# Performance work log

Hardware: AMD Instinct MI355X
Metric: run time of the kernel (lower is better)

The kernel has to match this reference:

```python
import jax, jax.numpy as jnp
import numpy as np

B, N, K, D, H, W = 16, 32, 32, 64, 128, 128  # batch, instances, dot_number, dot_dimension, fmap HxW
IMAGE_SIZE = 512.0
DOWN = 4.0
HID = 128


def setup_inputs() -> dict:
    key = jax.random.key(0)
    ks = jax.random.split(key, 16)
    s = 0.05
    x = jax.random.normal(ks[0], (B, 64, H, W), jnp.float32)
    mask_point = jax.random.uniform(ks[1], (B, N, K, 2), jnp.float32) * 511.0  # image-space coords
    point_mask = jnp.ones((B, N, K), jnp.int32)  # 1 = real point, 0 = zero-padded
    return {
        "x": x,
        "mask_point": mask_point,
        "point_mask": point_mask,
        "conv1_w": jax.random.normal(ks[2], (64, 64, 3, 3), jnp.float32) * s,
        "conv1_b": jnp.zeros((64,), jnp.float32),
        "conv2_w": jax.random.normal(ks[3], (D, 64), jnp.float32) * s,
        "conv2_b": jnp.full((D,), -2.19, jnp.float32),  # bias_fill with bias_value
        "Wih_e": jax.random.normal(ks[4], (4 * HID, D), jnp.float32) * s,
        "Whh_e": jax.random.normal(ks[5], (4 * HID, HID), jnp.float32) * s,
        "bih_e": jnp.zeros((4 * HID,), jnp.float32),
        "bhh_e": jnp.zeros((4 * HID,), jnp.float32),
        "Wih_d": jax.random.normal(ks[6], (4 * HID, HID), jnp.float32) * s,
        "Whh_d": jax.random.normal(ks[7], (4 * HID, HID), jnp.float32) * s,
        "bih_d": jnp.zeros((4 * HID,), jnp.float32),
        "bhh_d": jnp.zeros((4 * HID,), jnp.float32),
        "W1": jax.random.normal(ks[8], (64, HID), jnp.float32) * s,
        "b1": jnp.zeros((64,), jnp.float32),
        "W2": jax.random.normal(ks[9], (2, 64), jnp.float32) * s,
        "b2": jnp.zeros((2,), jnp.float32),
    }


def _lstm(seq, Wih, Whh, bih, bhh, h0, c0):
    # seq: [T, Bflat, in]; PyTorch gate order i, f, g, o
    bias = bih + bhh
    def step(carry, xt):
        h, c = carry
        g = xt @ Wih.T + h @ Whh.T + bias
        i, f, gg, o = jnp.split(g, 4, axis=-1)
        c = jax.nn.sigmoid(f) * c + jax.nn.sigmoid(i) * jnp.tanh(gg)
        h = jax.nn.sigmoid(o) * jnp.tanh(c)
        return (h, c), h
    (hT, cT), ys = jax.lax.scan(step, (h0, c0), seq)
    return ys, (hT, cT)


def reference(x, mask_point, point_mask, conv1_w, conv1_b, conv2_w, conv2_b,
              Wih_e, Whh_e, bih_e, bhh_e, Wih_d, Whh_d, bih_d, bhh_d,
              W1, b1, W2, b2):
    # SingleHead extraction: 3x3 conv -> ReLU -> 1x1 conv
    feat = jax.lax.conv_general_dilated(
        x, conv1_w, (1, 1), 'SAME',
        dimension_numbers=('NCHW', 'OIHW', 'NCHW')) + conv1_b[None, :, None, None]
    feat = jax.nn.relu(feat)
    fmap = jnp.einsum('bchw,dc->bdhw', feat, conv2_w) + conv2_b[None, :, None, None]
    xf = fmap.reshape(B, D, H * W)

    # keypoint index math (vectorized version of the nested python loops)
    pts = jnp.minimum(mask_point / DOWN, 127.0)        # [B,N,K,2] feature-map coords
    gt = pts * DOWN                                     # gt_keypoints
    flat = (pts[..., 1] * (IMAGE_SIZE / DOWN) + pts[..., 0]).astype(jnp.int32)  # [B,N,K]

    # gather dot features; zero padding where point_mask == 0
    dots = jax.vmap(lambda f, idx: f.T[idx])(xf, flat)  # [B,N,K,D]
    dots = dots * point_mask[..., None].astype(dots.dtype)

    seq = dots.reshape(B * N, K, D).transpose(1, 0, 2)  # [K, B*N, D] (time-major)
    h0 = jnp.zeros((B * N, HID), seq.dtype)
    enc, (h, c) = _lstm(seq, Wih_e, Whh_e, bih_e, bhh_e, h0, h0)
    dec, _ = _lstm(enc, Wih_d, Whh_d, bih_d, bhh_d, h, c)

    y = jax.nn.relu(dec @ W1.T + b1) @ W2.T + b2        # [K, B*N, 2]
    kp = y.transpose(1, 0, 2).reshape(B, N, K, 2)
    return kp, gt
```

## Files before the change

### kernel.cpp

```cpp
#include <hip/hip_runtime.h>
#include <stdint.h>

#define NSEQ 512
#define HIDN 128

#define OFF_FEIH   0
#define OFF_BIAS_E 65536
#define OFF_BIAS_D 67584
#define OFF_W1P    69632
#define OFF_W2P    143360
#define OFF_FLAT   151552
#define OFF_W1H    217088
#define OFF_FEHH   233472
#define OFF_FDIH8  364544
#define OFF_FDHH8  430080
#define OFF_W2T    495616
#define OFF_W1F8   504832
#define OFF_DOTS   (1024*1024)
#define OFF_XT     (4*1024*1024)
#define WS_NEED_XT ((size_t)(4*1024*1024) + (size_t)16*128*128*64 + 1024)

typedef _Float16 h2f __attribute__((ext_vector_type(2)));
typedef _Float16 f16x8 __attribute__((ext_vector_type(8)));
typedef float    f32x4 __attribute__((ext_vector_type(4)));

static __device__ __forceinline__ h2f u2h(uint32_t u) {
  union { uint32_t u; h2f h; } v; v.u = u; return v.h;
}

#if __has_builtin(__builtin_amdgcn_fdot2)
static __device__ __forceinline__ float fdot2_(uint32_t a, uint32_t b, float c) {
  return __builtin_amdgcn_fdot2(u2h(a), u2h(b), c, false);
}
#else
static __device__ __forceinline__ float fdot2_(uint32_t a, uint32_t b, float c) {
  h2f x = u2h(a), y = u2h(b);
  return c + (float)x.x * (float)y.x + (float)x.y * (float)y.y;
}
#endif

static __device__ __forceinline__ uint32_t packh(float a, float b) {
  union { _Float16 h[2]; uint32_t u; } v;
  v.h[0] = (_Float16)a; v.h[1] = (_Float16)b; return v.u;
}
static __device__ __forceinline__ float sig_(float x) {
  return 1.0f / (1.0f + __expf(-x));
}
static __device__ __forceinline__ float tanh_(float x) {
  return 1.0f - 2.0f / (1.0f + __expf(2.0f * x));
}

static __device__ __forceinline__ uint32_t f2e4m3_sw(float f) {
  union { float f; uint32_t u; } v; v.f = f;
  uint32_t s = (v.u >> 24) & 0x80u;
  float af = fabsf(f);
  if (af == 0.0f) return s;
  if (af >= 448.0f) return s | 0x7Eu;
  int e; float m = frexpf(af, &e);
  int E = e + 6;
  float mant = m * 2.0f - 1.0f;
  int mm = (int)(mant * 8.0f + 0.5f);
  if (mm == 8) { mm = 0; ++E; }
  if (E < 1) {
    int sm = (int)(af * 512.0f + 0.5f);
    return s | (uint32_t)(sm > 7 ? 7 : sm);
  }
  if (E > 15) return s | 0x7Eu;
  return s | ((uint32_t)E << 3) | (uint32_t)mm;
}
static __device__ __forceinline__ uint32_t pk4_fp8(float a, float b, float c, float d) {
#if __has_builtin(__builtin_amdgcn_cvt_pk_fp8_f32)
  int r = __builtin_amdgcn_cvt_pk_fp8_f32(a, b, 0, false);
  r = __builtin_amdgcn_cvt_pk_fp8_f32(c, d, r, true);
  return (uint32_t)r;
#else
  return f2e4m3_sw(a) | (f2e4m3_sw(b) << 8) | (f2e4m3_sw(c) << 16) | (f2e4m3_sw(d) << 24);
#endif
}
static __device__ __forceinline__ uint8_t f8_(float v) {
#if __has_builtin(__builtin_amdgcn_cvt_pk_fp8_f32)
  return (uint8_t)(__builtin_amdgcn_cvt_pk_fp8_f32(v, 0.f, 0, false) & 0xFF);
#else
  return (uint8_t)f2e4m3_sw(v);
#endif
}
static __device__ __forceinline__ long u2l(uint2 v) {
  union { uint2 v; long l; } x; x.v = v; return x.l;
}
static __device__ __forceinline__ uint2 ldg_frag8(const uint2* p) {
  uint2 r;
  asm volatile("global_load_dwordx2 %0, %1, off" : "=v"(r) : "v"(p));
  return r;
}
static __device__ __forceinline__ void frag_fence() {
  asm volatile("s_waitcnt vmcnt(0)" ::: "memory");
  __builtin_amdgcn_sched_barrier(0);
}

static __device__ void prep_body(int idx,
    const float* Wih_e, const float* Whh_e,
    const float* bih_e, const float* bhh_e,
    const float* Wih_d, const float* Whh_d,
    const float* bih_d, const float* bhh_d,
    const float* w1, const float* w2, const float* W1,
    const float* mask_point, float* out_gt, int* flat,
    char* ws, int w1_order) {
  float*    bias_e = (float*)(ws + OFF_BIAS_E);
  float*    bias_d = (float*)(ws + OFF_BIAS_D);
  uint32_t* w1p    = (uint32_t*)(ws + OFF_W1P);
  uint32_t* w2p    = (uint32_t*)(ws + OFF_W2P);
  uint32_t* W1h    = (uint32_t*)(ws + OFF_W1H);
  uint32_t* w2t    = (uint32_t*)(ws + OFF_W2T);
  uint32_t* w1f8   = (uint32_t*)(ws + OFF_W1F8);

  if (idx < 16384) {
    int j2 = idx & 3, lane = (idx >> 2) & 63, kt = (idx >> 8) & 1, gt = idx >> 9;
    int g = gt*16 + (lane & 15);
    int k = kt*32 + ((lane >> 4) & 3)*8 + 2*j2;
    ((uint32_t*)(ws + OFF_FEIH))[idx] = packh(Wih_e[g*64 + k], Wih_e[g*64 + k + 1]);
    return;
  }
  idx -= 16384;
  if (idx < 512) { bias_e[idx] = bih_e[idx] + bhh_e[idx]; return; }
  idx -= 512;
  if (idx < 512) { bias_d[idx] = bih_d[idx] + bhh_d[idx]; return; }
  idx -= 512;
  if (idx < 288*64) {
    int i2 = idx >> 6, c = idx & 63;
    if (w1_order) {
      int tap = i2 >> 5, cin = (i2 & 31) * 2;
      w1p[idx] = packh(w1[c*576 + cin*9 + tap], w1[c*576 + (cin+1)*9 + tap]);
    } else {
      w1p[idx] = packh(w1[c*576 + 2*i2], w1[c*576 + 2*i2 + 1]);
    }
    return;
  }
  idx -= 288*64;
  if (idx < 32*64) {
    int c2 = idx >> 6, d = idx & 63;
    w2p[idx] = packh(w2[d*64 + 2*c2], w2[d*64 + 2*c2 + 1]);
    return;
  }
  idx -= 32*64;
  if (idx < 64*64) {
    int k2 = idx >> 6, j = idx & 63;
    W1h[idx] = packh(W1[j*128 + 2*k2], W1[j*128 + 2*k2 + 1]);
    return;
  }
  idx -= 64*64;
  if (idx < 32768) {
    int j2 = idx & 3, lane = (idx >> 2) & 63, kt = (idx >> 8) & 3, gt = idx >> 10;
    int g = gt*16 + (lane & 15);
    int k = kt*32 + ((lane >> 4) & 3)*8 + 2*j2;
    ((uint32_t*)(ws + OFF_FEHH))[idx] = packh(Whh_e[g*128 + k], Whh_e[g*128 + k + 1]);
    return;
  }
  idx -= 32768;
  if (idx < 16384) {
    int half = idx & 1, lane = (idx >> 1) & 63, kt = (idx >> 7) & 3, gt = idx >> 9;
    int g = gt*16 + (lane & 15);
    int kb = kt*32 + ((lane >> 4) & 3)*8 + half*4;
    const float* W = Wih_d;
    ((uint32_t*)(ws + OFF_FDIH8))[(((gt*4 + kt)*64 + lane) << 1) | half] =
        pk4_fp8(W[g*128 + kb], W[g*128 + kb + 1], W[g*128 + kb + 2], W[g*128 + kb + 3]);
    return;
  }
  idx -= 16384;
  if (idx < 16384) {
    int half = idx & 1, lane = (idx >> 1) & 63, kt = (idx >> 7) & 3, gt = idx >> 9;
    int g = gt*16 + (lane & 15);
    int kb = kt*32 + ((lane >> 4) & 3)*8 + half*4;
    const float* W = Whh_d;
    ((uint32_t*)(ws + OFF_FDHH8))[(((gt*4 + kt)*64 + lane) << 1) | half] =
        pk4_fp8(W[g*128 + kb], W[g*128 + kb + 1], W[g*128 + kb + 2], W[g*128 + kb + 3]);
    return;
  }
  idx -= 16384;
  if (idx < 64*36) {
    int d = idx / 36, c2 = idx - (idx/36)*36;
    w2t[idx] = (c2 < 32) ? packh(w2[d*64 + 2*c2], w2[d*64 + 2*c2 + 1]) : 0u;
    return;
  }
  idx -= 64*36;
  if (idx < 64*144) {
    int c = idx / 144, j = idx - (idx/144)*144;
    int tap = j >> 4, cin0 = (j & 15) * 4;
    w1f8[idx] = pk4_fp8(w1[c*576 + (cin0+0)*9 + tap] * 16.0f,
                        w1[c*576 + (cin0+1)*9 + tap] * 16.0f,
                        w1[c*576 + (cin0+2)*9 + tap] * 16.0f,
                        w1[c*576 + (cin0+3)*9 + tap] * 16.0f);
    return;
  }
  idx -= 64*144;
  if (idx < 16384) {
    float mx = mask_point[idx*2 + 0];
    float my = mask_point[idx*2 + 1];
    float fx = fminf(mx * 0.25f, 127.0f);
    float fy = fminf(my * 0.25f, 127.0f);
    out_gt[idx*2 + 0] = fx * 4.0f;
    out_gt[idx*2 + 1] = fy * 4.0f;
    flat[idx] = (int)(__fmaf_rn(fy, 128.0f, fx));
    return;
  }
}
#define PREP_TOTAL (16384 + 512 + 512 + 288*64 + 32*64 + 64*64 + 32768 + 16384 + 16384 + 64*36 + 64*144 + 16384)
#define PREP_BLOCKS ((PREP_TOTAL + 255) / 256)

__global__ __launch_bounds__(256) void prep_kernel(
    const float* Wih_e, const float* Whh_e, const float* bih_e, const float* bhh_e,
    const float* Wih_d, const float* Whh_d, const float* bih_d, const float* bhh_d,
    const float* w1, const float* w2, const float* W1,
    const float* mask_point, float* out_gt, int* flat, char* ws, int w1_order) {
  prep_body(blockIdx.x * 256 + threadIdx.x,
            Wih_e, Whh_e, bih_e, bhh_e, Wih_d, Whh_d, bih_d, bhh_d,
            w1, w2, W1, mask_point, out_gt, flat, ws, w1_order);
}

__global__ __launch_bounds__(256, 2) void transpose_prep_kernel(
    const float* x, uint32_t* xT8,
    const float* Wih_e, const float* Whh_e, const float* bih_e, const float* bhh_e,
    const float* Wih_d, const float* Whh_d, const float* bih_d, const float* bhh_d,
    const float* w1, const float* w2, const float* W1,
    const float* mask_point, float* out_gt, int* flat, char* ws) {
  __shared__ float lds[64][257];
  int bid = blockIdx.x;
  if (bid >= 1024) {
    prep_body((bid - 1024) * 256 + threadIdx.x,
              Wih_e, Whh_e, bih_e, bhh_e, Wih_d, Whh_d, bih_d, bhh_d,
              w1, w2, W1, mask_point, out_gt, flat, ws, 1);
    return;
  }
  int xt = bid & 3, yt = (bid >> 2) & 15, b = bid >> 6;
  int x0 = xt * 32, y0 = yt * 8;
  int tx = threadIdx.x & 31, ty = threadIdx.x >> 5;
  #pragma unroll 8
  for (int c = 0; c < 64; ++c)
    lds[c][ty*32 + tx] = x[((b*64 + c)*128 + (y0 + ty))*128 + (x0 + tx)];
  __syncthreads();
  #pragma unroll 8
  for (int r = 0; r < 16; ++r) {
    int i = threadIdx.x + 256*r;
    int c4 = i & 15, pos = i >> 4;
    int yy = pos >> 5, xx = pos & 31;
    uint32_t v = pk4_fp8(lds[c4*4+0][pos], lds[c4*4+1][pos],
                         lds[c4*4+2][pos], lds[c4*4+3][pos]);
    xT8[((b*128 + y0 + yy)*128 + (x0 + xx))*16 + c4] = v;
  }
}

__global__ __launch_bounds__(512, 2) void conv_mfma8_kernel(
    const uint32_t* xT8, const int* point_mask,
    const float* conv1_b, const float* conv2_b,
    const char* ws_ro, _Float16* dots_h, const int* flat) {
  __shared__ __attribute__((aligned(16))) uint32_t w1s8[64*146];
  __shared__ __attribute__((aligned(16))) uint32_t patch8[32*146];
  __shared__ __attribute__((aligned(16))) uint32_t t1s[32*36];

  const uint32_t* w1f8 = (const uint32_t*)(ws_ro + OFF_W1F8);
  const uint32_t* w2t  = (const uint32_t*)(ws_ro + OFF_W2T);
  int tid  = threadIdx.x;
  int lane = tid & 63, wave = tid >> 6;
  int r = wave & 3, g = wave >> 2;
  int cl = lane & 15, lgrp = lane >> 4;

  #pragma unroll
  for (int i = tid; i < 64*144; i += 512) {
    int c = i / 144, j = i - c*144;
    w1s8[c*146 + j] = w1f8[i];
  }

  uint4 a2[2];
  #pragma unroll
  for (int kt = 0; kt < 2; ++kt)
    a2[kt] = *(const uint4*)&w2t[(r*16 + cl)*36 + kt*16 + lgrp*4];

  float4 b1r = *(const float4*)&conv1_b[r*16 + lgrp*4];
  float4 b2v = *(const float4*)&conv2_b[r*16 + lgrp*4];
  f32x4 b1v = {b1r.x*16.f, b1r.y*16.f, b1r.z*16.f, b1r.w*16.f};

  for (int it = 0; it < 2; ++it) {
    int p0 = blockIdx.x * 64 + it * 32;
    __syncthreads();
    #pragma unroll
    for (int rr = 0; rr < 9; ++rr) {
      int u = tid + 512*rr;
      int slot = u / 144, j = u - slot*144;
      int tap = j >> 4, c4 = j & 15;
      int p = p0 + slot;
      int fl = flat[p];
      int hh = fl >> 7, ww = fl & 127;
      int b = p >> 10;
      int dy = tap / 3, dx = tap - dy*3;
      int yy = hh + dy - 1, xx = ww + dx - 1;
      uint32_t v = 0u;
      if (yy >= 0 && yy < 128 && xx >= 0 && xx < 128)
        v = xT8[((b*128 + yy)*128 + xx)*16 + c4];
      patch8[slot*146 + j] = v;
    }
    __syncthreads();

    f32x4 acc = b1v;
    #pragma unroll
    for (int kt = 0; kt < 18; ++kt) {
      long af = u2l(*(const uint2*)&w1s8[(r*16 + cl)*146 + kt*8 + lgrp*2]);
      long bf = u2l(*(const uint2*)&patch8[(g*16 + cl)*146 + kt*8 + lgrp*2]);
      acc = __builtin_amdgcn_mfma_f32_16x16x32_fp8_fp8(af, bf, acc, 0, 0, 0);
    }
    {
      int trow = (g*16 + cl)*36 + r*8 + lgrp*2;
      t1s[trow]     = packh(fmaxf(acc[0], 0.f) * 0.0625f, fmaxf(acc[1], 0.f) * 0.0625f);
      t1s[trow + 1] = packh(fmaxf(acc[2], 0.f) * 0.0625f, fmaxf(acc[3], 0.f) * 0.0625f);
    }
    __syncthreads();

    f32x4 acc2 = {b2v.x, b2v.y, b2v.z, b2v.w};
    #pragma unroll
    for (int kt = 0; kt < 2; ++kt) {
      f16x8 af; __builtin_memcpy(&af, &a2[kt], 16);
      f16x8 bf = *(const f16x8*)&t1s[(g*16 + cl)*36 + kt*16 + lgrp*4];
      acc2 = __builtin_amdgcn_mfma_f32_16x16x32_f16(af, bf, acc2, 0, 0, 0);
    }
    {
      int p = p0 + g*16 + cl;
      float m = (float)point_mask[p];
      int kk = p & 31, bn = p >> 5;
      int d0 = r*16 + lgrp*4;
      uint2 o;
      o.x = packh(acc2[0]*m, acc2[1]*m);
      o.y = packh(acc2[2]*m, acc2[3]*m);
      *(uint2*)&dots_h[(size_t)(kk*NSEQ + bn)*64 + d0] = o;
    }
  }
}

__global__ __launch_bounds__(256, 2) void conv_gather_kernel(
    const float* x, const int* point_mask,
    const float* conv1_b, const float* conv2_b,
    const char* ws_ro, _Float16* dots_h, const int* flat) {
  __shared__ uint32_t w1s[64*292];
  __shared__ uint32_t patch2[4*288];
  __shared__ uint32_t tl2[4*32];

  const uint32_t* w1p = (const uint32_t*)(ws_ro + OFF_W1P);
  const uint32_t* w2p = (const uint32_t*)(ws_ro + OFF_W2P);
  int tid = threadIdx.x;
  for (int i = tid; i < 288*64; i += 256) {
    int i2 = i >> 6, cc = i & 63;
    w1s[cc*292 + i2] = w1p[i];
  }

  int q = tid >> 6, c = tid & 63;
  float c1b = conv1_b[c], c2b = conv2_b[c];

  for (int g = 0; g < 8; ++g) {
    int p0 = blockIdx.x * 32 + g * 4;
    __syncthreads();
    #pragma unroll
    for (int r = 0; r < 9; ++r) {
      int l = tid + 256*r;
      int slot = l / 576;
      int within = l - slot*576;
      int cp = within / 9;
      int tap = within - cp*9;
      int p = p0 + slot;
      int fl = flat[p];
      int hh = fl >> 7, ww = fl & 127;
      int b = p >> 10;
      int yy = hh + tap/3 - 1, xx = ww + tap%3 - 1;
      float v = 0.0f;
      if (yy >= 0 && yy < 128 && xx >= 0 && xx < 128)
        v = x[((b*64 + cp)*128 + yy)*128 + xx];
      ((_Float16*)patch2)[l] = (_Float16)v;
    }
    __syncthreads();

    float a0 = c1b, a1 = 0.f, a2 = 0.f, a3 = 0.f;
    int cbase = c * 292, pbase = q * 288;
    #pragma unroll 4
    for (int i2 = 0; i2 < 288; i2 += 4) {
      a0 = fdot2_(w1s[cbase + i2+0], patch2[pbase + i2+0], a0);
      a1 = fdot2_(w1s[cbase + i2+1], patch2[pbase + i2+1], a1);
      a2 = fdot2_(w1s[cbase + i2+2], patch2[pbase + i2+2], a2);
      a3 = fdot2_(w1s[cbase + i2+3], patch2[pbase + i2+3], a3);
    }
    float t1 = fmaxf((a0 + a1) + (a2 + a3), 0.0f);
    ((_Float16*)tl2)[q*64 + c] = (_Float16)t1;

    float acc2 = c2b;
    #pragma unroll
    for (int c2i = 0; c2i < 32; ++c2i)
      acc2 = fdot2_(w2p[c2i*64 + c], tl2[q*32 + c2i], acc2);
    int p = p0 + q;
    acc2 *= (float)point_mask[p];
    int k = p & 31, bn = p >> 5;
    dots_h[(k*NSEQ + bn)*64 + c] = (_Float16)acc2;
  }
}

__global__ __launch_bounds__(512, 2) void lstm_head_kernel(
    const char* ws_ro,
    const float* b1, const float* W2, const float* b2,
    float* out_kp) {
  const f16x8* feih   = (const f16x8*)(ws_ro + OFF_FEIH);
  const f16x8* fehh   = (const f16x8*)(ws_ro + OFF_FEHH);
  const uint2* fdih8  = (const uint2*)(ws_ro + OFF_FDIH8);
  const uint2* fdhh8  = (const uint2*)(ws_ro + OFF_FDHH8);
  const float* bias_e = (const float*)(ws_ro + OFF_BIAS_E);
  const float* bias_d = (const float*)(ws_ro + OFF_BIAS_D);
  const uint32_t* dots_u = (const uint32_t*)(ws_ro + OFF_DOTS);
  const uint32_t* W1h = (const uint32_t*)(ws_ro + OFF_W1H);

  __shared__ __attribute__((aligned(16))) uint32_t xs[2][32][32];
  __shared__ __attribute__((aligned(16))) uint32_t enc8[2][32][32];
  __shared__ __attribute__((aligned(16))) uint32_t dech2[2][32][64];
  __shared__ __attribute__((aligned(16))) uint32_t hb2[2][64];
  __shared__ __attribute__((aligned(16))) uint32_t hb8[2][32];
  __shared__ __attribute__((aligned(16))) float    gb[2][512];
  __shared__ float hidf[64][65];

  int tid  = threadIdx.x;
  int lane = tid & 63, wave = tid >> 6;
  int col  = lane & 15, lgrp = lane >> 4;
  int sb   = col & 1;
  int bn0  = blockIdx.x * 2;

  int s_nl = tid >> 7, u_nl = tid & 127;
  float c_reg = 0.0f;

  for (int i = tid; i < 2048; i += 512) {
    int s = i >> 10, rem = i & 1023, t = rem >> 5, k2 = rem & 31;
    xs[s][t][k2] = dots_u[(t*NSEQ + bn0 + s)*32 + k2];
  }

  f16x8 ax[4][2], ae[4][4];
  #pragma unroll
  for (int g0 = 0; g0 < 4; ++g0) {
    #pragma unroll
    for (int kt = 0; kt < 2; ++kt)
      ax[g0][kt] = feih[((wave*4 + g0)*2 + kt)*64 + lane];
    #pragma unroll
    for (int kt = 0; kt < 4; ++kt)
      ae[g0][kt] = fehh[((wave*4 + g0)*4 + kt)*64 + lane];
  }

  float be0 = bias_e[u_nl],       be1 = bias_e[128 + u_nl];
  float be2 = bias_e[256 + u_nl], be3 = bias_e[384 + u_nl];

  if (tid < 128) hb2[tid >> 6][tid & 63] = 0u;
  __syncthreads();

  const f16x8 bzero = {};

  for (int t = 0; t < 32; ++t) {
    f16x8 bx[2], bf[4];
    #pragma unroll
    for (int kt = 0; kt < 2; ++kt)
      bx[kt] = *(const f16x8*)&xs[sb][t][kt*16 + lgrp*4];
    #pragma unroll
    for (int kt = 0; kt < 4; ++kt) {
      if (col < 2) bf[kt] = *(const f16x8*)&hb2[col][kt*16 + lgrp*4];
      else         bf[kt] = bzero;
    }
    #pragma unroll
    for (int g0 = 0; g0 < 4; ++g0) {
      f32x4 acc = {0.f, 0.f, 0.f, 0.f};
      #pragma unroll
      for (int kt = 0; kt < 2; ++kt)
        acc = __builtin_amdgcn_mfma_f32_16x16x32_f16(ax[g0][kt], bx[kt], acc, 0, 0, 0);
      #pragma unroll
      for (int kt = 0; kt < 4; ++kt)
        acc = __builtin_amdgcn_mfma_f32_16x16x32_f16(ae[g0][kt], bf[kt], acc, 0, 0, 0);
      if (col < 2)
        *(f32x4*)&gb[col][(wave*4 + g0)*16 + lgrp*4] = acc;
    }
    __syncthreads();
    if (tid < 256) {
      float ig = sig_ (gb[s_nl][u_nl]       + be0);
      float fg = sig_ (gb[s_nl][128 + u_nl] + be1);
      float gg = tanh_(gb[s_nl][256 + u_nl] + be2);
      float og = sig_ (gb[s_nl][384 + u_nl] + be3);
      c_reg = fg * c_reg + ig * gg;
      float hh = og * tanh_(c_reg);
      ((_Float16*)&hb2[s_nl][0])[u_nl] = (_Float16)hh;
      ((uint8_t*)&enc8[s_nl][t][0])[u_nl] = f8_(hh);
    }
    __syncthreads();
  }

  if (tid < 256) {
    float hv = (float)((_Float16*)&hb2[s_nl][0])[u_nl];
    ((uint8_t*)&hb8[s_nl][0])[u_nl] = f8_(hv);
  }

  uint2 dih8[4][4], dhh8[4][4];
  #pragma unroll
  for (int g0 = 0; g0 < 4; ++g0)
    #pragma unroll
    for (int kt = 0; kt < 4; ++kt) {
      dih8[g0][kt] = ldg_frag8(&fdih8[((wave*4 + g0)*4 + kt)*64 + lane]);
      dhh8[g0][kt] = ldg_frag8(&fdhh8[((wave*4 + g0)*4 + kt)*64 + lane]);
    }
  frag_fence();
  float bdi = 0.f, bdf = 0.f, bdg = 0.f, bdo = 0.f;
  if (tid < 256) {
    bdi = bias_d[u_nl];       bdf = bias_d[128 + u_nl];
    bdg = bias_d[256 + u_nl]; bdo = bias_d[384 + u_nl];
  }
  __syncthreads();

  for (int t = 0; t < 32; ++t) {
    long bx[4], bh[4];
    #pragma unroll
    for (int kt = 0; kt < 4; ++kt) {
      if (col < 2) {
        bx[kt] = u2l(*(const uint2*)&enc8[col][t][kt*8 + lgrp*2]);
        bh[kt] = u2l(*(const uint2*)&hb8[col][kt*8 + lgrp*2]);
      } else { bx[kt] = 0; bh[kt] = 0; }
    }
    #pragma unroll
    for (int g0 = 0; g0 < 4; ++g0) {
      f32x4 acc = {0.f, 0.f, 0.f, 0.f};
      #pragma unroll
      for (int kt = 0; kt < 4; ++kt)
        acc = __builtin_amdgcn_mfma_f32_16x16x32_fp8_fp8(
            u2l(dih8[g0][kt]), bx[kt], acc, 0, 0, 0);
      #pragma unroll
      for (int kt = 0; kt < 4; ++kt)
        acc = __builtin_amdgcn_mfma_f32_16x16x32_fp8_fp8(
            u2l(dhh8[g0][kt]), bh[kt], acc, 0, 0, 0);
      if (col < 2)
        *(f32x4*)&gb[col][(wave*4 + g0)*16 + lgrp*4] = acc;
    }
    __syncthreads();
    if (tid < 256) {
      float ig = sig_ (gb[s_nl][u_nl]       + bdi);
      float fg = sig_ (gb[s_nl][128 + u_nl] + bdf);
      float gg = tanh_(gb[s_nl][256 + u_nl] + bdg);
      float og = sig_ (gb[s_nl][384 + u_nl] + bdo);
      c_reg = fg * c_reg + ig * gg;
      float hh = og * tanh_(c_reg);
      ((uint8_t*)&hb8[s_nl][0])[u_nl] = f8_(hh);
      ((_Float16*)&dech2[s_nl][t][0])[u_nl] = (_Float16)hh;
    }
    __syncthreads();
  }

  {
    int j = tid & 63, w = tid >> 6;
    float acc[8];
    #pragma unroll
    for (int m = 0; m < 8; ++m) acc[m] = b1[j];
    #pragma unroll 8
    for (int k = 0; k < 64; ++k) {
      uint32_t wv = W1h[k*64 + j];
      #pragma unroll
      for (int m = 0; m < 8; ++m) {
        int st = w + 8*m;
        acc[m] = fdot2_(wv, dech2[st >> 5][st & 31][k], acc[m]);
      }
    }
    #pragma unroll
    for (int m = 0; m < 8; ++m) {
      int st = w + 8*m;
      hidf[st][j] = fmaxf(acc[m], 0.0f);
    }
  }
  __syncthreads();
  if (tid < 128) {
    int st = tid >> 1, e = tid & 1;
    float acc = b2[e];
    #pragma unroll 16
    for (int j = 0; j < 64; ++j) acc += W2[e*64 + j] * hidf[st][j];
    int s = st >> 5, t = st & 31;
    out_kp[((bn0 + s)*32 + t)*2 + e] = acc;
  }
}

extern "C" void kernel_launch(void* const* d_in, const int* in_sizes, int n_in,
                              void* d_out, int out_size, void* d_ws, size_t ws_size,
                              hipStream_t stream) {
  const float* x          = (const float*)d_in[0];
  const float* mask_point = (const float*)d_in[1];
  const int*   point_mask = (const int*)d_in[2];
  const float* conv1_w    = (const float*)d_in[3];
  const float* conv1_b    = (const float*)d_in[4];
  const float* conv2_w    = (const float*)d_in[5];
  const float* conv2_b    = (const float*)d_in[6];
  const float* Wih_e      = (const float*)d_in[7];
  const float* Whh_e      = (const float*)d_in[8];
  const float* bih_e      = (const float*)d_in[9];
  const float* bhh_e      = (const float*)d_in[10];
  const float* Wih_d      = (const float*)d_in[11];
  const float* Whh_d      = (const float*)d_in[12];
  const float* bih_d      = (const float*)d_in[13];
  const float* bhh_d      = (const float*)d_in[14];
  const float* W1         = (const float*)d_in[15];
  const float* b1         = (const float*)d_in[16];
  const float* W2         = (const float*)d_in[17];
  const float* b2         = (const float*)d_in[18];

  float* out = (float*)d_out;
  char*  ws  = (char*)d_ws;

  const bool use_xt = (ws_size >= WS_NEED_XT);

  if (use_xt) {
    transpose_prep_kernel<<<1024 + PREP_BLOCKS, 256, 0, stream>>>(
        x, (uint32_t*)(ws + OFF_XT),
        Wih_e, Whh_e, bih_e, bhh_e, Wih_d, Whh_d, bih_d, bhh_d,
        conv1_w, conv2_w, W1, mask_point, out + 32768, (int*)(ws + OFF_FLAT), ws);
    conv_mfma8_kernel<<<256, 512, 0, stream>>>(
        (const uint32_t*)(ws + OFF_XT), point_mask, conv1_b, conv2_b,
        ws, (_Float16*)(ws + OFF_DOTS), (const int*)(ws + OFF_FLAT));
  } else {
    prep_kernel<<<PREP_BLOCKS, 256, 0, stream>>>(
        Wih_e, Whh_e, bih_e, bhh_e, Wih_d, Whh_d, bih_d, bhh_d,
        conv1_w, conv2_w, W1, mask_point, out + 32768, (int*)(ws + OFF_FLAT),
        ws, 1);
    conv_gather_kernel<<<512, 256, 0, stream>>>(
        x, point_mask, conv1_b, conv2_b,
        ws, (_Float16*)(ws + OFF_DOTS), (const int*)(ws + OFF_FLAT));
  }

  lstm_head_kernel<<<256, 512, 0, stream>>>(ws, b1, W2, b2, out);
}
```

Measured before the change: 106.1 us.

## Fuse conv gather kernel with LSTM head kernel, keeping dots in LDS

Merges the fp8 MFMA conv/gather kernel and the LSTM+MLP head into one kernel. Each block computes the 64 dot features for its two sequences and writes them straight into shared memory instead of a global dots buffer, then runs the encoder/decoder LSTM and head. Shared memory regions are aliased between the phases. This removes one kernel launch and the global round trip for the dots tensor, at the cost of higher LDS and register pressure in a single kernel. The LSTM weight fragments are now loaded only after the conv phase rather than overlapped with it.

After: 103.5 us. -2.5%, faster.

```diff
diff --git a/kernel.cpp b/kernel.cpp
--- a/kernel.cpp
+++ b/kernel.cpp
@@ -248,88 +248,265 @@
   }
 }
 
-__global__ __launch_bounds__(512, 2) void conv_mfma8_kernel(
+#define SM_W1S8   0
+#define SM_PATCH  37376
+#define SM_T1S    56064
+#define SM_DECH2  0
+#define SM_HIDF   16384
+#define SM_BYTES  60672
+
+__global__ __launch_bounds__(512, 2) void conv_lstm_kernel(
     const uint32_t* xT8, const int* point_mask,
     const float* conv1_b, const float* conv2_b,
-    const char* ws_ro, _Float16* dots_h, const int* flat) {
-  __shared__ __attribute__((aligned(16))) uint32_t w1s8[64*146];
-  __shared__ __attribute__((aligned(16))) uint32_t patch8[32*146];
-  __shared__ __attribute__((aligned(16))) uint32_t t1s[32*36];
-
+    const char* ws_ro, const int* flat,
+    const float* b1, const float* W2, const float* b2,
+    float* out_kp) {
+  __shared__ __attribute__((aligned(16))) char smem[SM_BYTES];
+  __shared__ __attribute__((aligned(16))) uint32_t xs[2][32][32];
+  __shared__ __attribute__((aligned(16))) uint32_t enc8[2][32][32];
+  __shared__ __attribute__((aligned(16))) uint32_t hb2[2][64];
+  __shared__ __attribute__((aligned(16))) uint32_t hb8[2][32];
+  __shared__ __attribute__((aligned(16))) float    gb[2][512];
+
+  const f16x8* feih   = (const f16x8*)(ws_ro + OFF_FEIH);
+  const f16x8* fehh   = (const f16x8*)(ws_ro + OFF_FEHH);
+  const uint2* fdih8  = (const uint2*)(ws_ro + OFF_FDIH8);
+  const uint2* fdhh8  = (const uint2*)(ws_ro + OFF_FDHH8);
+  const float* bias_e = (const float*)(ws_ro + OFF_BIAS_E);
+  const float* bias_d = (const float*)(ws_ro + OFF_BIAS_D);
+  const uint32_t* W1h = (const uint32_t*)(ws_ro + OFF_W1H);
   const uint32_t* w1f8 = (const uint32_t*)(ws_ro + OFF_W1F8);
   const uint32_t* w2t  = (const uint32_t*)(ws_ro + OFF_W2T);
+
   int tid  = threadIdx.x;
   int lane = tid & 63, wave = tid >> 6;
-  int r = wave & 3, g = wave >> 2;
   int cl = lane & 15, lgrp = lane >> 4;
 
+  {
+    uint32_t* w1s8   = (uint32_t*)(smem + SM_W1S8);
+    uint32_t* patch8 = (uint32_t*)(smem + SM_PATCH);
+    uint32_t* t1s    = (uint32_t*)(smem + SM_T1S);
+    int r = wave & 3, g = wave >> 2;
+
+    #pragma unroll
+    for (int i = tid; i < 64*144; i += 512) {
+      int c = i / 144, j = i - c*144;
+      w1s8[c*146 + j] = w1f8[i];
+    }
+
+    uint4 a2[2];
+    #pragma unroll
+    for (int kt = 0; kt < 2; ++kt)
+      a2[kt] = *(const uint4*)&w2t[(r*16 + cl)*36 + kt*16 + lgrp*4];
+
+    float4 b1r = *(const float4*)&conv1_b[r*16 + lgrp*4];
+    float4 b2v = *(const float4*)&conv2_b[r*16 + lgrp*4];
+    f32x4 b1v = {b1r.x*16.f, b1r.y*16.f, b1r.z*16.f, b1r.w*16.f};
+
+    for (int it = 0; it < 2; ++it) {
+      int p0 = blockIdx.x * 64 + it * 32;
+      __syncthreads();
+      #pragma unroll
+      for (int rr = 0; rr < 9; ++rr) {
+        int u = tid + 512*rr;
+        int slot = u / 144, j = u - slot*144;
+        int tap = j >> 4, c4 = j & 15;
+        int p = p0 + slot;
+        int fl = flat[p];
+        int hh = fl >> 7, ww = fl & 127;
+        int b = p >> 10;
+        int dy = tap / 3, dx = tap - dy*3;
+        int yy = hh + dy - 1, xx = ww + dx - 1;
+        uint32_t v = 0u;
+        if (yy >= 0 && yy < 128 && xx >= 0 && xx < 128)
+          v = xT8[((b*128 + yy)*128 + xx)*16 + c4];
+        patch8[slot*146 + j] = v;
+      }
+      __syncthreads();
+
+      f32x4 acc = b1v;
+      #pragma unroll
+      for (int kt = 0; kt < 18; ++kt) {
+        long af = u2l(*(const uint2*)&w1s8[(r*16 + cl)*146 + kt*8 + lgrp*2]);
+        long bf = u2l(*(const uint2*)&patch8[(g*16 + cl)*146 + kt*8 + lgrp*2]);
+        acc = __builtin_amdgcn_mfma_f32_16x16x32_fp8_fp8(af, bf, acc, 0, 0, 0);
+      }
+      {
+        int trow = (g*16 + cl)*36 + r*8 + lgrp*2;
+        t1s[trow]     = packh(fmaxf(acc[0], 0.f) * 0.0625f, fmaxf(acc[1], 0.f) * 0.0625f);
+        t1s[trow + 1] = packh(fmaxf(acc[2], 0.f) * 0.0625f, fmaxf(acc[3], 0.f) * 0.0625f);
+      }
+      __syncthreads();
+
+      f32x4 acc2 = {b2v.x, b2v.y, b2v.z, b2v.w};
+      #pragma unroll
+      for (int kt = 0; kt < 2; ++kt) {
+        f16x8 af; __builtin_memcpy(&af, &a2[kt], 16);
+        f16x8 bf = *(const f16x8*)&t1s[(g*16 + cl)*36 + kt*16 + lgrp*4];
+        acc2 = __builtin_amdgcn_mfma_f32_16x16x32_f16(af, bf, acc2, 0, 0, 0);
+      }
+      {
+        int p = p0 + g*16 + cl;
+        float m = (float)point_mask[p];
+        uint2 o;
+        o.x = packh(acc2[0]*m, acc2[1]*m);
+        o.y = packh(acc2[2]*m, acc2[3]*m);
+        *(uint2*)&xs[it][g*16 + cl][r*8 + lgrp*2] = o;
+      }
+    }
+  }
+  __syncthreads();
+
+  uint32_t* dech2 = (uint32_t*)(smem + SM_DECH2);
+  float*    hidf  = (float*)(smem + SM_HIDF);
+
+  int col = cl;
+  int sb  = col & 1;
+  int bn0 = blockIdx.x * 2;
+  int s_nl = tid >> 7, u_nl = tid & 127;
+  float c_reg = 0.0f;
+
+  f16x8 ax[4][2], ae[4][4];
   #pragma unroll
-  for (int i = tid; i < 64*144; i += 512) {
-    int c = i / 144, j = i - c*144;
-    w1s8[c*146 + j] = w1f8[i];
-  }
-
-  uint4 a2[2];
+  for (int g0 = 0; g0 < 4; ++g0) {
+    #pragma unroll
+    for (int kt = 0; kt < 2; ++kt)
+      ax[g0][kt] = feih[((wave*4 + g0)*2 + kt)*64 + lane];
+    #pragma unroll
+    for (int kt = 0; kt < 4; ++kt)
+      ae[g0][kt] = fehh[((wave*4 + g0)*4 + kt)*64 + lane];
+  }
+
+  float be0 = bias_e[u_nl],       be1 = bias_e[128 + u_nl];
+  float be2 = bias_e[256 + u_nl], be3 = bias_e[384 + u_nl];
+
+  if (tid < 128) hb2[tid >> 6][tid & 63] = 0u;
+  __syncthreads();
+
+  const f16x8 bzero = {};
+
+  for (int t = 0; t < 32; ++t) {
+    f16x8 bx[2], bf[4];
+    #pragma unroll
+    for (int kt = 0; kt < 2; ++kt)
+      bx[kt] = *(const f16x8*)&xs[sb][t][kt*16 + lgrp*4];
+    #pragma unroll
+    for (int kt = 0; kt < 4; ++kt) {
+      if (col < 2) bf[kt] = *(const f16x8*)&hb2[col][kt*16 + lgrp*4];
+      else         bf[kt] = bzero;
+    }
+    #pragma unroll
+    for (int g0 = 0; g0 < 4; ++g0) {
+      f32x4 acc = {0.f, 0.f, 0.f, 0.f};
+      #pragma unroll
+      for (int kt = 0; kt < 2; ++kt)
+        acc = __builtin_amdgcn_mfma_f32_16x16x32_f16(ax[g0][kt], bx[kt], acc, 0, 0, 0);
+      #pragma unroll
+      for (int kt = 0; kt < 4; ++kt)
+        acc = __builtin_amdgcn_mfma_f32_16x16x32_f16(ae[g0][kt], bf[kt], acc, 0, 0, 0);
+      if (col < 2)
+        *(f32x4*)&gb[col][(wave*4 + g0)*16 + lgrp*4] = acc;
+    }
+    __syncthreads();
+    if (tid < 256) {
+      float ig = sig_ (gb[s_nl][u_nl]       + be0);
+      float fg = sig_ (gb[s_nl][128 + u_nl] + be1);
+      float gg = tanh_(gb[s_nl][256 + u_nl] + be2);
+      float og = sig_ (gb[s_nl][384 + u_nl] + be3);
+      c_reg = fg * c_reg + ig * gg;
+      float hh = og * tanh_(c_reg);
+      ((_Float16*)&hb2[s_nl][0])[u_nl] = (_Float16)hh;
+      ((uint8_t*)&enc8[s_nl][t][0])[u_nl] = f8_(hh);
+    }
+    __syncthreads();
+  }
+
+  if (tid < 256) {
+    float hv = (float)((_Float16*)&hb2[s_nl][0])[u_nl];
+    ((uint8_t*)&hb8[s_nl][0])[u_nl] = f8_(hv);
+  }
+
+  uint2 dih8[4][4], dhh8[4][4];
   #pragma unroll
-  for (int kt = 0; kt < 2; ++kt)
-    a2[kt] = *(const uint4*)&w2t[(r*16 + cl)*36 + kt*16 + lgrp*4];
-
-  float4 b1r = *(const float4*)&conv1_b[r*16 + lgrp*4];
-  float4 b2v = *(const float4*)&conv2_b[r*16 + lgrp*4];
-  f32x4 b1v = {b1r.x*16.f, b1r.y*16.f, b1r.z*16.f, b1r.w*16.f};
-
-  for (int it = 0; it < 2; ++it) {
-    int p0 = blockIdx.x * 64 + it * 32;
-    __syncthreads();
-    #pragma unroll
-    for (int rr = 0; rr < 9; ++rr) {
-      int u = tid + 512*rr;
-      int slot = u / 144, j = u - slot*144;
-      int tap = j >> 4, c4 = j & 15;
-      int p = p0 + slot;
-      int fl = flat[p];
-      int hh = fl >> 7, ww = fl & 127;
-      int b = p >> 10;
-      int dy = tap / 3, dx = tap - dy*3;
-      int yy = hh + dy - 1, xx = ww + dx - 1;
-      uint32_t v = 0u;
-      if (yy >= 0 && yy < 128 && xx >= 0 && xx < 128)
-        v = xT8[((b*128 + yy)*128 + xx)*16 + c4];
-      patch8[slot*146 + j] = v;
-    }
-    __syncthreads();
-
-    f32x4 acc = b1v;
-    #pragma unroll
-    for (int kt = 0; kt < 18; ++kt) {
-      long af = u2l(*(const uint2*)&w1s8[(r*16 + cl)*146 + kt*8 + lgrp*2]);
-      long bf = u2l(*(const uint2*)&patch8[(g*16 + cl)*146 + kt*8 + lgrp*2]);
-      acc = __builtin_amdgcn_mfma_f32_16x16x32_fp8_fp8(af, bf, acc, 0, 0, 0);
-    }
-    {
-      int trow = (g*16 + cl)*36 + r*8 + lgrp*2;
-      t1s[trow]     = packh(fmaxf(acc[0], 0.f) * 0.0625f, fmaxf(acc[1], 0.f) * 0.0625f);
-      t1s[trow + 1] = packh(fmaxf(acc[2], 0.f) * 0.0625f, fmaxf(acc[3], 0.f) * 0.0625f);
-    }
-    __syncthreads();
-
-    f32x4 acc2 = {b2v.x, b2v.y, b2v.z, b2v.w};
-    #pragma unroll
-    for (int kt = 0; kt < 2; ++kt) {
-      f16x8 af; __builtin_memcpy(&af, &a2[kt], 16);
-      f16x8 bf = *(const f16x8*)&t1s[(g*16 + cl)*36 + kt*16 + lgrp*4];
-      acc2 = __builtin_amdgcn_mfma_f32_16x16x32_f16(af, bf, acc2, 0, 0, 0);
-    }
-    {
-      int p = p0 + g*16 + cl;
-      float m = (float)point_mask[p];
-      int kk = p & 31, bn = p >> 5;
-      int d0 = r*16 + lgrp*4;
-      uint2 o;
-      o.x = packh(acc2[0]*m, acc2[1]*m);
-      o.y = packh(acc2[2]*m, acc2[3]*m);
-      *(uint2*)&dots_h[(size_t)(kk*NSEQ + bn)*64 + d0] = o;
-    }
+  for (int g0 = 0; g0 < 4; ++g0)
+    #pragma unroll
+    for (int kt = 0; kt < 4; ++kt) {
+      dih8[g0][kt] = ldg_frag8(&fdih8[((wave*4 + g0)*4 + kt)*64 + lane]);
+      dhh8[g0][kt] = ldg_frag8(&fdhh8[((wave*4 + g0)*4 + kt)*64 + lane]);
+    }
+  frag_fence();
+  float bdi = 0.f, bdf = 0.f, bdg = 0.f, bdo = 0.f;
+  if (tid < 256) {
+    bdi = bias_d[u_nl];       bdf = bias_d[128 + u_nl];
+    bdg = bias_d[256 + u_nl]; bdo = bias_d[384 + u_nl];
+  }
+  __syncthreads();
+
+  for (int t = 0; t < 32; ++t) {
+    long bx[4], bh[4];
+    #pragma unroll
+    for (int kt = 0; kt < 4; ++kt) {
+      if (col < 2) {
+        bx[kt] = u2l(*(const uint2*)&enc8[col][t][kt*8 + lgrp*2]);
+        bh[kt] = u2l(*(const uint2*)&hb8[col][kt*8 + lgrp*2]);
+      } else { bx[kt] = 0; bh[kt] = 0; }
+    }
+    #pragma unroll
+    for (int g0 = 0; g0 < 4; ++g0) {
+      f32x4 acc = {0.f, 0.f, 0.f, 0.f};
+      #pragma unroll
+      for (int kt = 0; kt < 4; ++kt)
+        acc = __builtin_amdgcn_mfma_f32_16x16x32_fp8_fp8(
+            u2l(dih8[g0][kt]), bx[kt], acc, 0, 0, 0);
+      #pragma unroll
+      for (int kt = 0; kt < 4; ++kt)
+        acc = __builtin_amdgcn_mfma_f32_16x16x32_fp8_fp8(
+            u2l(dhh8[g0][kt]), bh[kt], acc, 0, 0, 0);
+      if (col < 2)
+        *(f32x4*)&gb[col][(wave*4 + g0)*16 + lgrp*4] = acc;
+    }
+    __syncthreads();
+    if (tid < 256) {
+      float ig = sig_ (gb[s_nl][u_nl]       + bdi);
+      float fg = sig_ (gb[s_nl][128 + u_nl] + bdf);
+      float gg = tanh_(gb[s_nl][256 + u_nl] + bdg);
+      float og = sig_ (gb[s_nl][384 + u_nl] + bdo);
+      c_reg = fg * c_reg + ig * gg;
+      float hh = og * tanh_(c_reg);
+      ((uint8_t*)&hb8[s_nl][0])[u_nl] = f8_(hh);
+      ((_Float16*)&dech2[(s_nl*32 + t)*64])[u_nl] = (_Float16)hh;
+    }
+    __syncthreads();
+  }
+
+  {
+    int j = tid & 63, w = tid >> 6;
+    float acc[8];
+    #pragma unroll
+    for (int m = 0; m < 8; ++m) acc[m] = b1[j];
+    #pragma unroll 8
+    for (int k = 0; k < 64; ++k) {
+      uint32_t wv = W1h[k*64 + j];
+      #pragma unroll
+      for (int m = 0; m < 8; ++m) {
+        int st = w + 8*m;
+        acc[m] = fdot2_(wv, dech2[st*64 + k], acc[m]);
+      }
+    }
+    #pragma unroll
+    for (int m = 0; m < 8; ++m) {
+      int st = w + 8*m;
+      hidf[st*65 + j] = fmaxf(acc[m], 0.0f);
+    }
+  }
+  __syncthreads();
+  if (tid < 128) {
+    int st = tid >> 1, e = tid & 1;
+    float acc = b2[e];
+    #pragma unroll 16
+    for (int j = 0; j < 64; ++j) acc += W2[e*64 + j] * hidf[st*65 + j];
+    int s = st >> 5, t = st & 31;
+    out_kp[((bn0 + s)*32 + t)*2 + e] = acc;
   }
 }
 
@@ -397,7 +574,7 @@
   }
 }
 
-__global__ __launch_bounds__(512, 2) void lstm_head_kernel(
+__global__ __launch_bounds__(512, 2) void lstm_head_fb_kernel(
     const char* ws_ro,
     const float* b1, const float* W2, const float* b2,
     float* out_kp) {
@@ -423,7 +600,6 @@
   int col  = lane & 15, lgrp = lane >> 4;
   int sb   = col & 1;
   int bn0  = blockIdx.x * 2;
-
   int s_nl = tid >> 7, u_nl = tid & 127;
   float c_reg = 0.0f;
 
@@ -609,9 +785,9 @@
         x, (uint32_t*)(ws + OFF_XT),
         Wih_e, Whh_e, bih_e, bhh_e, Wih_d, Whh_d, bih_d, bhh_d,
         conv1_w, conv2_w, W1, mask_point, out + 32768, (int*)(ws + OFF_FLAT), ws);
-    conv_mfma8_kernel<<<256, 512, 0, stream>>>(
+    conv_lstm_kernel<<<256, 512, 0, stream>>>(
         (const uint32_t*)(ws + OFF_XT), point_mask, conv1_b, conv2_b,
-        ws, (_Float16*)(ws + OFF_DOTS), (const int*)(ws + OFF_FLAT));
+        ws, (const int*)(ws + OFF_FLAT), b1, W2, b2, out);
   } else {
     prep_kernel<<<PREP_BLOCKS, 256, 0, stream>>>(
         Wih_e, Whh_e, bih_e, bhh_e, Wih_d, Whh_d, bih_d, bhh_d,
@@ -620,7 +796,6 @@
     conv_gather_kernel<<<512, 256, 0, stream>>>(
         x, point_mask, conv1_b, conv2_b,
         ws, (_Float16*)(ws + OFF_DOTS), (const int*)(ws + OFF_FLAT));
-  }
-
-  lstm_head_kernel<<<256, 512, 0, stream>>>(ws, b1, W2, b2, out);
-}
+    lstm_head_fb_kernel<<<256, 512, 0, stream>>>(ws, b1, W2, b2, out);
+  }
+}
```
